# Optimization experiments

Hardware: AMD Instinct MI355X
Metric: run time of the kernel (lower is better)

The kernel has to match this reference:

```python
import jax, jax.numpy as jnp
import numpy as np

B, S, D = 4, 2048, 1024
H, HD = 16, 64            # num heads, head dim (H*HD == D)
FF = 4096                  # llama intermediate size
EPS = 1e-6
THETA = 10000.0


def rms_norm(x, w):
    v = jnp.mean(jnp.square(x), axis=-1, keepdims=True)
    return x * jax.lax.rsqrt(v + EPS) * w


def apply_rope(x, pos):
    # x: [B,H,S,HD]; HF llama rotate_half convention
    inv = 1.0 / (THETA ** (jnp.arange(0, HD, 2, dtype=jnp.float32) / HD))  # [HD/2]
    ang = pos[:, None].astype(jnp.float32) * inv[None, :]                   # [S,HD/2]
    cos = jnp.concatenate([jnp.cos(ang), jnp.cos(ang)], -1)[None, None]     # [1,1,S,HD]
    sin = jnp.concatenate([jnp.sin(ang), jnp.sin(ang)], -1)[None, None]
    x1, x2 = jnp.split(x, 2, axis=-1)
    return x * cos + jnp.concatenate([-x2, x1], axis=-1) * sin


def setup_inputs() -> dict:
    key = jax.random.key(0)
    ks = jax.random.split(key, 12)
    p = lambda k, shp: (0.02 * jax.random.normal(k, shp, dtype=jnp.float32))
    return {
        "chunk_hidden_states": jax.random.normal(ks[0], (B, S, D), dtype=jnp.float32),
        "Wq": p(ks[1], (D, D)),
        "Wk": p(ks[2], (D, D)),
        "Wv": p(ks[3], (D, D)),
        "Wo": p(ks[4], (D, D)),
        "ln1_w": jnp.ones((D,), dtype=jnp.float32),
        "ln2_w": jnp.ones((D,), dtype=jnp.float32),
        "Wgate": p(ks[5], (FF, D)),
        "Wup": p(ks[6], (FF, D)),
        "Wdown": p(ks[7], (D, FF)),
        "W_out": p(ks[8], (1024, D)),
        "b_out": jnp.zeros((1024,), dtype=jnp.float32),
    }


def reference(chunk_hidden_states, Wq, Wk, Wv, Wo, ln1_w, ln2_w,
              Wgate, Wup, Wdown, W_out, b_out):
    x = chunk_hidden_states                      # [B,S,D]
    pos = jnp.arange(S)

    # --- self attention block ---
    h = rms_norm(x, ln1_w)
    q = (h @ Wq.T).reshape(B, S, H, HD).transpose(0, 2, 1, 3)  # [B,H,S,HD]
    k = (h @ Wk.T).reshape(B, S, H, HD).transpose(0, 2, 1, 3)
    v = (h @ Wv.T).reshape(B, S, H, HD).transpose(0, 2, 1, 3)
    q = apply_rope(q, pos)
    k = apply_rope(k, pos)
    # attention_mask is None when the layer is called directly -> full (non-causal) attention
    scores = jnp.einsum("bhqd,bhkd->bhqk", q, k) / jnp.sqrt(jnp.float32(HD))
    attn = jax.nn.softmax(scores, axis=-1)
    ctx = jnp.einsum("bhqk,bhkd->bhqd", attn, v)             # [B,H,S,HD]
    ctx = ctx.transpose(0, 2, 1, 3).reshape(B, S, D)
    x = x + ctx @ Wo.T

    # --- MLP block (SwiGLU) ---
    h2 = rms_norm(x, ln2_w)
    mlp = (jax.nn.silu(h2 @ Wgate.T) * (h2 @ Wup.T)) @ Wdown.T
    x = x + mlp

    # --- output head ---
    logits = x @ W_out.T + b_out                 # [B,S,1024]
    return logits.reshape(-1, 8, 1024)
```

## Files before the change

### kernel.cpp

```cpp
#include <hip/hip_runtime.h>

#define TB 4
#define TS 2048
#define TD 1024
#define TH 16
#define THD 64
#define TFF 4096
#define TTOK (TB*TS)

typedef unsigned int  uint32;
typedef unsigned short u16;
typedef short s8v __attribute__((ext_vector_type(8)));
typedef short s4bf __attribute__((ext_vector_type(4)));
typedef float f4v __attribute__((ext_vector_type(4)));

#define BF16_MAGIC 0x3f803f80u

__device__ __forceinline__ u16 f2bf(float f){
    uint32 u = __float_as_uint(f);
    u += 0x7fffu + ((u >> 16) & 1u);
    return (u16)(u >> 16);
}
__device__ __forceinline__ float bf2f(u16 h){
    return __uint_as_float(((uint32)h) << 16);
}
__device__ __forceinline__ void gload_lds16(const void* g, void* l){
    __builtin_amdgcn_global_load_lds(
        (const __attribute__((address_space(1))) unsigned int*)g,
        (__attribute__((address_space(3))) unsigned int*)l,
        16, 0, 0);
}
__device__ __forceinline__ void bar(){
    asm volatile("" ::: "memory");
    __builtin_amdgcn_s_barrier();
    asm volatile("" ::: "memory");
}
#define WAITVM(N) asm volatile("s_waitcnt vmcnt(" #N ")" ::: "memory")

struct CvtDesc { const void* src; void* dst; int n; int mode; };
struct CvtArgs { CvtDesc d[13]; };

__global__ __launch_bounds__(256)
void cvt_all(CvtArgs a, const uint32* __restrict__ flag){
    const bool isbf = (*flag == BF16_MAGIC);
    CvtDesc dd = a.d[blockIdx.y];
    if (dd.mode == 2){
        float* cosT = (float*)dd.dst;
        float* sinT = cosT + TS*32;
        for (int i = blockIdx.x*256 + threadIdx.x; i < dd.n; i += 256*gridDim.x){
            int s = i >> 5, f = i & 31;
            double inv = pow(10000.0, -(double)f/32.0);
            double ang = (double)s * inv;
            cosT[i] = (float)cos(ang);
            sinT[i] = (float)sin(ang);
        }
        return;
    }
    int n4 = dd.n >> 2;
    if (dd.mode == 1){
        float* dst = (float*)dd.dst;
        for (int i = blockIdx.x*256 + threadIdx.x; i < n4; i += 256*gridDim.x){
            float4 v;
            if (isbf){
                ushort4 u = ((const ushort4*)dd.src)[i];
                v = make_float4(bf2f(u.x), bf2f(u.y), bf2f(u.z), bf2f(u.w));
            } else v = ((const float4*)dd.src)[i];
            ((float4*)dst)[i] = v;
        }
        return;
    }
    for (int i = blockIdx.x*256 + threadIdx.x; i < n4; i += 256*gridDim.x){
        ushort4 o;
        if (isbf) o = ((const ushort4*)dd.src)[i];
        else {
            float4 v = ((const float4*)dd.src)[i];
            o.x=f2bf(v.x); o.y=f2bf(v.y); o.z=f2bf(v.z); o.w=f2bf(v.w);
        }
        size_t di = i;
        if (dd.mode >= 3){
            int row = i >> 8, c4 = i & 255;
            int drow = ((row >> 6) << 7) + (row & 63) + ((dd.mode == 4) ? 64 : 0);
            di = (size_t)drow*256 + c4;
        }
        ((ushort4*)dd.dst)[di] = o;
    }
}

__global__ __launch_bounds__(256)
void rmsnorm_k(const float* __restrict__ x, const float* __restrict__ w, u16* __restrict__ out){
    int row = blockIdx.x, tid = threadIdx.x;
    float4 xv = ((const float4*)(x + (size_t)row*TD))[tid];
    float s = xv.x*xv.x + xv.y*xv.y + xv.z*xv.z + xv.w*xv.w;
    #pragma unroll
    for (int off = 32; off > 0; off >>= 1) s += __shfl_xor(s, off);
    __shared__ float red[4];
    if ((tid & 63) == 0) red[tid >> 6] = s;
    __syncthreads();
    float tot = red[0]+red[1]+red[2]+red[3];
    float rs = rsqrtf(tot * (1.0f/TD) + 1e-6f);
    float4 wv = ((const float4*)w)[tid];
    ushort4 o;
    o.x = f2bf(xv.x*rs*wv.x); o.y = f2bf(xv.y*rs*wv.y);
    o.z = f2bf(xv.z*rs*wv.z); o.w = f2bf(xv.w*rs*wv.w);
    ((ushort4*)(out + (size_t)row*TD))[tid] = o;
}

enum { EPI_ADDF32 = 1, EPI_OUT = 3, EPI_QKVROPE = 4, EPI_ADDBF16 = 5, EPI_GATEUP = 6 };

template<int EPI>
__global__ __launch_bounds__(256)
void gemm_bt(const u16* __restrict__ A, int lda,
             const u16* __restrict__ W, int ldw,
             int K,
             void* __restrict__ outp, int ldo,
             const float* __restrict__ bias,
             const uint32* __restrict__ flag,
             u16* __restrict__ q_out, u16* __restrict__ k_out, u16* __restrict__ vt_out,
             const float* __restrict__ cosT, const float* __restrict__ sinT,
             const float* __restrict__ resid)
{
    __shared__ __align__(16) u16 SMEM[2*128*64];
    u16* As = SMEM;
    u16* Bs = SMEM + 128*64;
    const int tid  = threadIdx.x;
    const int wave = tid >> 6;
    const int lane = tid & 63;
    const int nbx = gridDim.x;
    const int lin = blockIdx.y * nbx + blockIdx.x;
    const int swz = (lin & 7) * ((nbx * gridDim.y) >> 3) + (lin >> 3);
    const int tm = (swz / nbx) * 128;
    const int tn = (swz % nbx) * 128;
    const int wm = (wave >> 1) * 64;
    const int wn = (wave &  1) * 64;

    f4v acc[4][4] = {};

    const int srow8 = lane >> 3;
    const int ch    = lane & 7;
    const int lrow  = lane & 15;
    const int lq    = lane >> 4;

    const u16* Ag = A + (size_t)(tm + wave*32 + srow8)*lda + ((ch ^ srow8) << 3);
    const u16* Wg = W + (size_t)(tn + wave*32 + srow8)*ldw + ((ch ^ srow8) << 3);

    for (int k0 = 0; k0 < K; k0 += 64){
        __syncthreads();
        #pragma unroll
        for (int i8 = 0; i8 < 4; i8++){
            gload_lds16(Ag + (size_t)(i8*8)*lda + k0, As + (wave*32 + i8*8)*64);
            gload_lds16(Wg + (size_t)(i8*8)*ldw + k0, Bs + (wave*32 + i8*8)*64);
        }
        __syncthreads();

        #pragma unroll
        for (int kk = 0; kk < 2; kk++){
            s8v a[4], b[4];
            #pragma unroll
            for (int i = 0; i < 4; i++){
                int row = wm + i*16 + lrow;
                a[i] = *(const s8v*)(As + row*64 + (((kk*4 + lq) ^ (lrow & 7)) << 3));
            }
            #pragma unroll
            for (int j = 0; j < 4; j++){
                int row = wn + j*16 + lrow;
                b[j] = *(const s8v*)(Bs + row*64 + (((kk*4 + lq) ^ (lrow & 7)) << 3));
            }
            #pragma unroll
            for (int i = 0; i < 4; i++)
                #pragma unroll
                for (int j = 0; j < 4; j++)
                    acc[i][j] = __builtin_amdgcn_mfma_f32_16x16x32_bf16(a[i], b[j], acc[i][j], 0, 0, 0);
        }
    }

    if constexpr (EPI == EPI_QKVROPE){
        const int ncol0 = tn + wn;
        if (ncol0 < 2048){
            u16* dst = (ncol0 < 1024) ? q_out : k_out;
            const int cbase = ncol0 & 1023;
            #pragma unroll
            for (int i = 0; i < 4; i++){
                #pragma unroll
                for (int r = 0; r < 4; r++){
                    int row = tm + wm + i*16 + lq*4 + r;
                    int s = row & (TS-1);
                    #pragma unroll
                    for (int j = 0; j < 2; j++){
                        int d = j*16 + lrow;
                        float c  = cosT[s*32 + d];
                        float sn = sinT[s*32 + d];
                        float x1 = acc[i][j][r], x2 = acc[i][j+2][r];
                        dst[(size_t)row*TD + cbase + d]      = f2bf(x1*c - x2*sn);
                        dst[(size_t)row*TD + cbase + d + 32] = f2bf(x2*c + x1*sn);
                    }
                }
            }
        } else {
            #pragma unroll
            for (int i = 0; i < 4; i++)
                #pragma unroll
                for (int j = 0; j < 4; j++)
                    #pragma unroll
                    for (int r = 0; r < 4; r++){
                        int row = tm + wm + i*16 + lq*4 + r;
                        int col = ncol0 - 2048 + j*16 + lrow;
                        int bb = row >> 11, s = row & (TS-1);
                        int hh = col >> 6, hd = col & 63;
                        vt_out[((size_t)(bb*TH + hh)*THD + hd)*TS + s] = f2bf(acc[i][j][r]);
                    }
        }
        return;
    }

    bool obf = false;
    if (EPI == EPI_OUT) obf = (*flag == BF16_MAGIC);
    #pragma unroll
    for (int i = 0; i < 4; i++){
        #pragma unroll
        for (int j = 0; j < 4; j++){
            #pragma unroll
            for (int r = 0; r < 4; r++){
                int row = tm + wm + i*16 + lq*4 + r;
                int col = tn + wn + j*16 + lrow;
                size_t idx = (size_t)row*ldo + col;
                float val = acc[i][j][r];
                if constexpr (EPI == EPI_ADDF32){
                    float* o = (float*)outp;
                    o[idx] += val;
                } else if constexpr (EPI == EPI_ADDBF16){
                    ((u16*)outp)[idx] = f2bf(resid[idx] + val);
                } else {
                    float v2 = val + bias[col];
                    if (obf) ((u16*)outp)[idx] = f2bf(v2);
                    else     ((float*)outp)[idx] = v2;
                }
            }
        }
    }
}

template<int EPI>
__global__ __launch_bounds__(512, 2)
void gemm256(const u16* __restrict__ A, int lda,
             const u16* __restrict__ W, int ldw,
             int K,
             void* __restrict__ outp, int ldo,
             const float* __restrict__ resid)
{
    __shared__ __align__(16) u16 SM[2][2*256*64];
    const int tid  = threadIdx.x;
    const int wave = tid >> 6;
    const int lane = tid & 63;
    const int wm = wave >> 2;
    const int wn = wave & 3;
    const int lrow = lane & 15;
    const int lq   = lane >> 4;
    const int srow8 = lane >> 3;
    const int ch    = lane & 7;

    const int nbx = gridDim.x;
    const int lin = blockIdx.y * nbx + blockIdx.x;
    const int swz = (lin & 7) * ((nbx * gridDim.y) >> 3) + (lin >> 3);
    const int tm = (swz / nbx) * 256;
    const int tn = (swz % nbx) * 256;

    const int NT = K >> 6;

    const u16* Ag = A + (size_t)(tm + wave*8 + srow8)*lda + ((ch ^ srow8) << 3);
    const u16* Wg = W + (size_t)(tn + wave*8 + srow8)*ldw + ((ch ^ srow8) << 3);

    f4v acc[2][4][2][2] = {};
    s8v a[2][4];
    s8v b[2][2];

    auto stageA = [&](int bufi, int g, int t){
        size_t k0 = (size_t)t * 64;
        #pragma unroll
        for (int r = 0; r < 2; r++)
            gload_lds16(Ag + (size_t)(g*128 + r*64)*lda + k0,
                        &SM[bufi][(g*128 + r*64 + wave*8)*64]);
    };
    auto stageB = [&](int bufi, int h, int t){
        size_t k0 = (size_t)t * 64;
        #pragma unroll
        for (int r = 0; r < 2; r++)
            gload_lds16(Wg + (size_t)(h*128 + r*64)*ldw + k0,
                        &SM[bufi][256*64 + (h*128 + r*64 + wave*8)*64]);
    };
    auto ldA = [&](int bufi, int g){
        #pragma unroll
        for (int kk = 0; kk < 2; kk++)
            #pragma unroll
            for (int i = 0; i < 4; i++){
                int row = g*128 + wm*64 + i*16 + lrow;
                a[kk][i] = *(const s8v*)(&SM[bufi][row*64 + (((kk*4 + lq) ^ (lrow & 7)) << 3)]);
            }
    };
    auto ldB = [&](int bufi, int h){
        #pragma unroll
        for (int kk = 0; kk < 2; kk++)
            #pragma unroll
            for (int j = 0; j < 2; j++){
                int row = h*128 + wn*32 + j*16 + lrow;
                b[kk][j] = *(const s8v*)(&SM[bufi][256*64 + row*64 + (((kk*4 + lq) ^ (lrow & 7)) << 3)]);
            }
    };
    auto mmac = [&](int g, int h){
        __builtin_amdgcn_s_setprio(1);
        #pragma unroll
        for (int kk = 0; kk < 2; kk++)
            #pragma unroll
            for (int i = 0; i < 4; i++)
                #pragma unroll
                for (int j = 0; j < 2; j++)
                    acc[g][i][h][j] = __builtin_amdgcn_mfma_f32_16x16x32_bf16(
                        a[kk][i], b[kk][j], acc[g][i][h][j], 0, 0, 0);
        __builtin_amdgcn_s_setprio(0);
    };

    stageA(0,0,0); stageB(0,0,0); stageB(0,1,0); stageA(0,1,0);
    stageA(1,0,1); stageB(1,1,1); stageA(1,1,1);
    WAITVM(6); bar();

    for (int t = 0; t < NT-2; t++){
        const int buf = t & 1, nb = buf ^ 1;
        ldA(buf,0); ldB(buf,0);
        stageB(nb,0,t+1);
        bar(); mmac(0,0); bar();
        ldB(buf,1);
        stageA(buf,0,t+2);
        bar(); mmac(0,1); bar();
        ldA(buf,1);
        stageB(buf,1,t+2);
        bar(); mmac(1,1); bar();
        ldB(buf,0);
        stageA(buf,1,t+2);
        WAITVM(6);
        bar(); mmac(1,0); bar();
    }
    {
        const int buf = (NT-2) & 1, nb = buf ^ 1;
        ldA(buf,0); ldB(buf,0);
        stageB(nb,0,NT-1);
        bar(); mmac(0,0); bar();
        ldB(buf,1);
        bar(); mmac(0,1); bar();
        ldA(buf,1);
        bar(); mmac(1,1); bar();
        ldB(buf,0);
        WAITVM(0);
        bar(); mmac(1,0); bar();
    }
    {
        const int buf = (NT-1) & 1;
        ldA(buf,0); ldB(buf,0);
        bar(); mmac(0,0); bar();
        ldB(buf,1);
        bar(); mmac(0,1); bar();
        ldA(buf,1);
        bar(); mmac(1,1); bar();
        ldB(buf,0);
        bar(); mmac(1,0); bar();
    }

    if constexpr (EPI == EPI_GATEUP){
        bar();
        float* X = (float*)&SM[0][0];
        const int uw = wm*2 + (wn & 1);
        if (wn >= 2){
            #pragma unroll
            for (int g = 0; g < 2; g++)
            #pragma unroll
            for (int i = 0; i < 4; i++)
            #pragma unroll
            for (int h = 0; h < 2; h++)
            #pragma unroll
            for (int j = 0; j < 2; j++)
            #pragma unroll
            for (int r = 0; r < 4; r++)
                X[uw*8192 + (g*64 + i*16 + lq*4 + r)*64
                          + ((h*32 + j*16 + lrow) ^ (lq << 3))] = acc[g][i][h][j][r];
        }
        bar();
        if (wn < 2){
            u16* o = (u16*)outp;
            #pragma unroll
            for (int g = 0; g < 2; g++)
            #pragma unroll
            for (int i = 0; i < 4; i++)
            #pragma unroll
            for (int h = 0; h < 2; h++)
            #pragma unroll
            for (int j = 0; j < 2; j++)
            #pragma unroll
            for (int r = 0; r < 4; r++){
                float gv = acc[g][i][h][j][r];
                float uv = X[uw*8192 + (g*64 + i*16 + lq*4 + r)*64
                                     + ((h*32 + j*16 + lrow) ^ (lq << 3))];
                float mres = (gv / (1.0f + __expf(-gv))) * uv;
                int row = tm + g*128 + wm*64 + i*16 + lq*4 + r;
                int ff  = (tn >> 1) + h*64 + wn*32 + j*16 + lrow;
                o[(size_t)row*TFF + ff] = f2bf(mres);
            }
        }
        return;
    }

    if constexpr (EPI == EPI_ADDBF16){
        u16* o = (u16*)outp;
        #pragma unroll
        for (int g = 0; g < 2; g++)
        #pragma unroll
        for (int i = 0; i < 4; i++)
        #pragma unroll
        for (int h = 0; h < 2; h++)
        #pragma unroll
        for (int j = 0; j < 2; j++)
        #pragma unroll
        for (int r = 0; r < 4; r++){
            int row = tm + g*128 + wm*64 + i*16 + lq*4 + r;
            int col = tn + h*128 + wn*32 + j*16 + lrow;
            size_t idx = (size_t)row*ldo + col;
            o[idx] = f2bf(resid[idx] + acc[g][i][h][j][r]);
        }
        return;
    }
}

__global__ __launch_bounds__(256, 2)
void flash_attn_mfma(const u16* __restrict__ qg, const u16* __restrict__ kg,
                     const u16* __restrict__ vt, u16* __restrict__ ctx)
{
    __shared__ u16 Qs[128*64];
    __shared__ u16 Ks[64*64];
    __shared__ u16 VT2[8*64*8];
    const int tid  = threadIdx.x;
    const int wave = tid >> 6;
    const int lane = tid & 63;
    const int qd   = lane >> 4;
    const int mm   = lane & 15;
    const int lin = blockIdx.y * 16 + blockIdx.x;
    const int swz = (lin & 7) * 128 + (lin >> 3);
    const int b  = swz >> 8, h = (swz >> 4) & 15;
    const int q0 = (swz & 15) * 128;
    const size_t tok0 = (size_t)b * TS;
    const u16* vtb = vt + (size_t)(b*TH + h)*THD*TS;
    const int rl = lane >> 3, ch = lane & 7;

    #pragma unroll
    for (int i = 0; i < 4; i++){
        int row = wave*32 + i*8 + rl;
        const u16* gp = qg + (tok0 + q0 + row)*TD + h*THD + ((ch ^ (row & 7)) << 3);
        gload_lds16(gp, Qs + (wave*32 + i*8)*64);
    }
    __syncthreads();

    s8v qf[2][2];
    #pragma unroll
    for (int ct = 0; ct < 2; ct++){
        int row = wave*32 + ct*16 + mm;
        #pragma unroll
        for (int hs = 0; hs < 2; hs++)
            qf[ct][hs] = *(const s8v*)(Qs + row*64 + (((hs*4 + qd) ^ (row & 7)) << 3));
    }

    f4v acc[2][4] = {};
    float mrun[2] = {-3.0e38f, -3.0e38f};
    float lrun[2] = {0.0f, 0.0f};
    const float SC2 = 0.18033688011112042f;

    for (int kt = 0; kt < TS/64; kt++){
        __syncthreads();
        #pragma unroll
        for (int i = 0; i < 2; i++){
            int row = wave*16 + i*8 + rl;
            const u16* gp = kg + (tok0 + kt*64 + row)*TD + h*THD + ((ch ^ (row & 7)) << 3);
            gload_lds16(gp, Ks + (wave*16 + i*8)*64);
        }
        #pragma unroll
        for (int ii = 0; ii < 2; ii++){
            int kb = wave*2 + ii;
            const u16* gp = vtb + (size_t)lane*TS + kt*64 + kb*8;
            gload_lds16(gp, VT2 + kb*64*8);
        }
        __syncthreads();

        f4v sc[4][2] = {};
        #pragma unroll
        for (int rt = 0; rt < 4; rt++){
            int row = rt*16 + mm;
            #pragma unroll
            for (int hs = 0; hs < 2; hs++){
                s8v kf = *(const s8v*)(Ks + row*64 + (((hs*4 + qd) ^ (row & 7)) << 3));
                #pragma unroll
                for (int ct = 0; ct < 2; ct++)
                    sc[rt][ct] = __builtin_amdgcn_mfma_f32_16x16x32_bf16(kf, qf[ct][hs], sc[rt][ct], 0, 0, 0);
            }
        }
        union VU { s4bf h[2]; s8v v; };
        VU vf8[2][4];
        #pragma unroll
        for (int t = 0; t < 2; t++){
            int kbA = 4*t + (qd >> 1);
            #pragma unroll
            for (int n = 0; n < 4; n++){
                const u16* base = VT2 + ((16*n + mm)*8) + ((qd & 1) * 4);
                vf8[t][n].h[0] = *(const s4bf*)(base + kbA*512);
                vf8[t][n].h[1] = *(const s4bf*)(base + (kbA+2)*512);
            }
        }

        #pragma unroll
        for (int ct = 0; ct < 2; ct++){
            float mx = sc[0][ct][0];
            #pragma unroll
            for (int rt = 0; rt < 4; rt++)
                #pragma unroll
                for (int r = 0; r < 4; r++)
                    mx = fmaxf(mx, sc[rt][ct][r]);
            mx = fmaxf(mx, __shfl_xor(mx, 16));
            mx = fmaxf(mx, __shfl_xor(mx, 32));
            float mn = fmaxf(mrun[ct], mx * SC2);
            float alpha = __builtin_amdgcn_exp2f(mrun[ct] - mn);
            mrun[ct] = mn;
            float ls = 0.0f;
            uint32 pk[4][2];
            #pragma unroll
            for (int rt = 0; rt < 4; rt++){
                float p0 = __builtin_amdgcn_exp2f(fmaf(sc[rt][ct][0], SC2, -mn));
                float p1 = __builtin_amdgcn_exp2f(fmaf(sc[rt][ct][1], SC2, -mn));
                float p2 = __builtin_amdgcn_exp2f(fmaf(sc[rt][ct][2], SC2, -mn));
                float p3 = __builtin_amdgcn_exp2f(fmaf(sc[rt][ct][3], SC2, -mn));
                ls += (p0 + p1) + (p2 + p3);
                pk[rt][0] = (__float_as_uint(p0) >> 16) | (__float_as_uint(p1) & 0xFFFF0000u);
                pk[rt][1] = (__float_as_uint(p2) >> 16) | (__float_as_uint(p3) & 0xFFFF0000u);
            }
            ls += __shfl_xor(ls, 16);
            ls += __shfl_xor(ls, 32);
            lrun[ct] = lrun[ct]*alpha + ls;
            #pragma unroll
            for (int r = 0; r < 4; r++){
                float ar = __shfl(alpha, (lane & 48) + qd*4 + r);
                #pragma unroll
                for (int n = 0; n < 4; n++)
                    acc[ct][n][r] *= ar;
            }
            #pragma unroll
            for (int t = 0; t < 2; t++){
                union { uint32 u[4]; s8v s; } pu;
                pu.u[0] = pk[2*t][0];   pu.u[1] = pk[2*t][1];
                pu.u[2] = pk[2*t+1][0]; pu.u[3] = pk[2*t+1][1];
                #pragma unroll
                for (int n = 0; n < 4; n++)
                    acc[ct][n] = __builtin_amdgcn_mfma_f32_16x16x32_bf16(pu.s, vf8[t][n].v, acc[ct][n], 0, 0, 0);
            }
        }
    }
    #pragma unroll
    for (int ct = 0; ct < 2; ct++){
        float rli = 1.0f / lrun[ct];
        #pragma unroll
        for (int r = 0; r < 4; r++){
            float ir = __shfl(rli, (lane & 48) + qd*4 + r);
            int row = q0 + wave*32 + ct*16 + qd*4 + r;
            u16* op = ctx + (tok0 + row)*TD + h*THD + mm;
            #pragma unroll
            for (int n = 0; n < 4; n++)
                op[16*n] = f2bf(acc[ct][n][r] * ir);
        }
    }
}

extern "C" void kernel_launch(void* const* d_in, const int* in_sizes, int n_in,
                              void* d_out, int out_size, void* d_ws, size_t ws_size,
                              hipStream_t stream)
{
    const uint32* flag = (const uint32*)d_in[5];
    char* ws = (char*)d_ws;
    size_t off = 0;
    auto alloc = [&](size_t bytes) -> void* {
        void* p = ws + off;
        off += (bytes + 255) & ~(size_t)255;
        return p;
    };
    float* xf   = (float*)alloc((size_t)TTOK*TD*4);
    u16*   hbf  = (u16*)  alloc((size_t)TTOK*TD*2);
    u16*   qb   = (u16*)  alloc((size_t)TTOK*TD*2);
    u16*   kb   = (u16*)  alloc((size_t)TTOK*TD*2);
    u16*   cb   = (u16*)  alloc((size_t)TTOK*TD*2);
    u16*   vt   = (u16*)  alloc((size_t)TTOK*TD*2);
    u16*   wqkv = (u16*)  alloc((size_t)3*TD*TD*2);
    u16*   wo   = (u16*)  alloc((size_t)TD*TD*2);
    u16*   wfu  = (u16*)  alloc((size_t)2*TFF*TD*2);
    u16*   wd   = (u16*)  alloc((size_t)TD*TFF*2);
    u16*   wou  = (u16*)  alloc((size_t)TD*TD*2);
    float* ln1  = (float*)alloc(TD*4);
    float* ln2  = (float*)alloc(TD*4);
    float* bo   = (float*)alloc(TD*4);
    float* cosT = (float*)alloc((size_t)TS*32*4*2);
    float* sinT = cosT + TS*32;
    u16*   mbuf = qb;
    (void)ws_size; (void)in_sizes; (void)n_in; (void)out_size;

    CvtArgs ca;
    ca.d[0]  = { d_in[0],  xf,            TTOK*TD, 1 };
    ca.d[1]  = { d_in[1],  wqkv,          TD*TD,   0 };
    ca.d[2]  = { d_in[2],  wqkv + (size_t)TD*TD,   TD*TD, 0 };
    ca.d[3]  = { d_in[3],  wqkv + (size_t)2*TD*TD, TD*TD, 0 };
    ca.d[4]  = { d_in[4],  wo,            TD*TD,   0 };
    ca.d[5]  = { d_in[7],  wfu,           TFF*TD,  3 };
    ca.d[6]  = { d_in[8],  wfu,           TFF*TD,  4 };
    ca.d[7]  = { d_in[9],  wd,            TD*TFF,  0 };
    ca.d[8]  = { d_in[10], wou,           TD*TD,   0 };
    ca.d[9]  = { d_in[5],  ln1,           TD,      1 };
    ca.d[10] = { d_in[6],  ln2,           TD,      1 };
    ca.d[11] = { d_in[11], bo,            TD,      1 };
    ca.d[12] = { nullptr,  cosT,          TS*32,   2 };
    cvt_all<<<dim3(256,13),256,0,stream>>>(ca, flag);

    rmsnorm_k<<<TTOK,256,0,stream>>>(xf, ln1, hbf);
    gemm_bt<EPI_QKVROPE><<<dim3(24, TTOK/128),256,0,stream>>>(
        hbf, TD, wqkv, TD, TD, nullptr, 0, nullptr, nullptr,
        qb, kb, vt, cosT, sinT, nullptr);
    flash_attn_mfma<<<dim3(TS/128, TB*TH),256,0,stream>>>(qb, kb, vt, cb);
    gemm_bt<EPI_ADDF32><<<dim3(TD/128, TTOK/128),256,0,stream>>>(
        cb, TD, wo, TD, TD, xf, TD, nullptr, nullptr,
        nullptr, nullptr, nullptr, nullptr, nullptr, nullptr);

    rmsnorm_k<<<TTOK,256,0,stream>>>(xf, ln2, hbf);
    gemm256<EPI_GATEUP><<<dim3(2*TFF/256, TTOK/256),512,0,stream>>>(
        hbf, TD, wfu, TD, TD, mbuf, TFF, nullptr);
    gemm_bt<EPI_ADDBF16><<<dim3(TD/128, TTOK/128),256,0,stream>>>(
        mbuf, TFF, wd, TFF, TFF, hbf, TD, nullptr, nullptr,
        nullptr, nullptr, nullptr, nullptr, nullptr, xf);

    gemm_bt<EPI_OUT><<<dim3(TD/128, TTOK/128),256,0,stream>>>(
        hbf, TD, wou, TD, TD, d_out, TD, bo, flag,
        nullptr, nullptr, nullptr, nullptr, nullptr, nullptr);
}
```

Before: 676.6 us.

## Double-buffer K/V tiles in flash attention and raise wave priority around MFMAs

The attention kernel now keeps two LDS buffers for K and V^T. It issues the global-to-LDS loads for the next key tile before computing on the current one, and replaces the two per-iteration barriers with a single wait-and-barrier at the end of each iteration. This is meant to hide global memory latency behind the MFMA and softmax work. It also wraps the MFMA sections in s_setprio and raises launch bounds to 3 blocks per CU. The extra LDS (about 32KB per block) and the register cap from the higher occupancy target could cause spills or limit residency.

```diff
diff --git a/kernel.cpp b/kernel.cpp
--- a/kernel.cpp
+++ b/kernel.cpp
@@ -427,13 +427,13 @@
     }
 }
 
-__global__ __launch_bounds__(256, 2)
+__global__ __launch_bounds__(256, 3)
 void flash_attn_mfma(const u16* __restrict__ qg, const u16* __restrict__ kg,
                      const u16* __restrict__ vt, u16* __restrict__ ctx)
 {
     __shared__ u16 Qs[128*64];
-    __shared__ u16 Ks[64*64];
-    __shared__ u16 VT2[8*64*8];
+    __shared__ u16 Ks[2][64*64];
+    __shared__ u16 VT2[2][8*64*8];
     const int tid  = threadIdx.x;
     const int wave = tid >> 6;
     const int lane = tid & 63;
@@ -447,12 +447,28 @@
     const u16* vtb = vt + (size_t)(b*TH + h)*THD*TS;
     const int rl = lane >> 3, ch = lane & 7;
 
+    auto stageKV = [&](int bufi, int kt2){
+        #pragma unroll
+        for (int i = 0; i < 2; i++){
+            int row = wave*16 + i*8 + rl;
+            const u16* gp = kg + (tok0 + kt2*64 + row)*TD + h*THD + ((ch ^ (row & 7)) << 3);
+            gload_lds16(gp, Ks[bufi] + (wave*16 + i*8)*64);
+        }
+        #pragma unroll
+        for (int ii = 0; ii < 2; ii++){
+            int kb = wave*2 + ii;
+            const u16* gp = vtb + (size_t)lane*TS + kt2*64 + kb*8;
+            gload_lds16(gp, VT2[bufi] + kb*64*8);
+        }
+    };
+
     #pragma unroll
     for (int i = 0; i < 4; i++){
         int row = wave*32 + i*8 + rl;
         const u16* gp = qg + (tok0 + q0 + row)*TD + h*THD + ((ch ^ (row & 7)) << 3);
         gload_lds16(gp, Qs + (wave*32 + i*8)*64);
     }
+    stageKV(0, 0);
     __syncthreads();
 
     s8v qf[2][2];
@@ -470,33 +486,23 @@
     const float SC2 = 0.18033688011112042f;
 
     for (int kt = 0; kt < TS/64; kt++){
-        __syncthreads();
-        #pragma unroll
-        for (int i = 0; i < 2; i++){
-            int row = wave*16 + i*8 + rl;
-            const u16* gp = kg + (tok0 + kt*64 + row)*TD + h*THD + ((ch ^ (row & 7)) << 3);
-            gload_lds16(gp, Ks + (wave*16 + i*8)*64);
-        }
-        #pragma unroll
-        for (int ii = 0; ii < 2; ii++){
-            int kb = wave*2 + ii;
-            const u16* gp = vtb + (size_t)lane*TS + kt*64 + kb*8;
-            gload_lds16(gp, VT2 + kb*64*8);
-        }
-        __syncthreads();
+        const int buf = kt & 1;
+        if (kt < TS/64 - 1) stageKV(buf ^ 1, kt + 1);
 
         f4v sc[4][2] = {};
+        __builtin_amdgcn_s_setprio(1);
         #pragma unroll
         for (int rt = 0; rt < 4; rt++){
             int row = rt*16 + mm;
             #pragma unroll
             for (int hs = 0; hs < 2; hs++){
-                s8v kf = *(const s8v*)(Ks + row*64 + (((hs*4 + qd) ^ (row & 7)) << 3));
+                s8v kf = *(const s8v*)(Ks[buf] + row*64 + (((hs*4 + qd) ^ (row & 7)) << 3));
                 #pragma unroll
                 for (int ct = 0; ct < 2; ct++)
                     sc[rt][ct] = __builtin_amdgcn_mfma_f32_16x16x32_bf16(kf, qf[ct][hs], sc[rt][ct], 0, 0, 0);
             }
         }
+        __builtin_amdgcn_s_setprio(0);
         union VU { s4bf h[2]; s8v v; };
         VU vf8[2][4];
         #pragma unroll
@@ -504,7 +510,7 @@
             int kbA = 4*t + (qd >> 1);
             #pragma unroll
             for (int n = 0; n < 4; n++){
-                const u16* base = VT2 + ((16*n + mm)*8) + ((qd & 1) * 4);
+                const u16* base = VT2[buf] + ((16*n + mm)*8) + ((qd & 1) * 4);
                 vf8[t][n].h[0] = *(const s4bf*)(base + kbA*512);
                 vf8[t][n].h[1] = *(const s4bf*)(base + (kbA+2)*512);
             }
@@ -545,6 +551,7 @@
                 for (int n = 0; n < 4; n++)
                     acc[ct][n][r] *= ar;
             }
+            __builtin_amdgcn_s_setprio(1);
             #pragma unroll
             for (int t = 0; t < 2; t++){
                 union { uint32 u[4]; s8v s; } pu;
@@ -554,6 +561,12 @@
                 for (int n = 0; n < 4; n++)
                     acc[ct][n] = __builtin_amdgcn_mfma_f32_16x16x32_bf16(pu.s, vf8[t][n].v, acc[ct][n], 0, 0, 0);
             }
+            __builtin_amdgcn_s_setprio(0);
+        }
+
+        if (kt < TS/64 - 1){
+            WAITVM(0);
+            bar();
         }
     }
     #pragma unroll
```

Result: no change. 675.1 us (-0.2%).
